# Kernel optimization log

Measured on AMD Instinct MI355X. Metric: run time of the kernel, lower is better.

## Reference

```python
import jax, jax.numpy as jnp
import numpy as np

N, E, D, H = 50000, 500000, 128, 8
DH = D // H  # per-head dim = int(out_dim // num_heads)
EPS_LN = 1e-5
EPS_BN = 1e-5


def _ln(x, g, b):
    m = x.mean(-1, keepdims=True)
    v = ((x - m) ** 2).mean(-1, keepdims=True)
    return (x - m) * jax.lax.rsqrt(v + EPS_LN) * g + b


def _bn(x, g, b):
    # BatchNorm1d, training-mode statistics (biased variance over the batch)
    m = x.mean(0)
    v = ((x - m) ** 2).mean(0)
    return (x - m) * jax.lax.rsqrt(v + EPS_BN) * g + b


def setup_inputs() -> dict:
    key = jax.random.key(0)
    ks = jax.random.split(key, 16)
    rn = lambda k, shape: (jax.random.normal(k, shape, jnp.float32) * 0.05)
    h = jax.random.normal(ks[0], (N, D), jnp.float32)
    src = jax.random.randint(ks[1], (E,), 0, N).astype(jnp.int32)
    # guarantee every node receives at least one message so z > 0 (no 0/0)
    dst = jnp.concatenate([jnp.arange(N, dtype=jnp.int32),
                           jax.random.randint(ks[2], (E - N,), 0, N).astype(jnp.int32)])
    return {
        "h": h, "src": src, "dst": dst,
        # per-node TransformerEncoder (seq_len == 1 subgraphs)
        "Win": rn(ks[3], (3 * D, D)), "bin": jnp.zeros((3 * D,), jnp.float32),
        "Wout": rn(ks[4], (D, D)), "bout": jnp.zeros((D,), jnp.float32),
        "Wte1": rn(ks[5], (4 * D, D)), "bte1": jnp.zeros((4 * D,), jnp.float32),
        "Wte2": rn(ks[6], (D, 4 * D)), "bte2": jnp.zeros((D,), jnp.float32),
        "ln1g": jnp.ones((D,), jnp.float32), "ln1b": jnp.zeros((D,), jnp.float32),
        "ln2g": jnp.ones((D,), jnp.float32), "ln2b": jnp.zeros((D,), jnp.float32),
        # graph multi-head attention projections (use_bias=False)
        "WQ": rn(ks[7], (D, D)), "WK": rn(ks[8], (D, D)), "WV": rn(ks[9], (D, D)),
        # node-wise FFN + batch norms
        "W1": rn(ks[10], (2 * D, D)), "b1": jnp.zeros((2 * D,), jnp.float32),
        "W2": rn(ks[11], (D, 2 * D)), "b2": jnp.zeros((D,), jnp.float32),
        "bn1g": jnp.ones((D,), jnp.float32), "bn1b": jnp.zeros((D,), jnp.float32),
        "bn2g": jnp.ones((D,), jnp.float32), "bn2b": jnp.zeros((D,), jnp.float32),
    }


def _forward(h, src, dst, Win, bin_, Wout, bout, Wte1, bte1, Wte2, bte2,
             ln1g, ln1b, ln2g, ln2b, WQ, WK, WV,
             W1, b1, W2, b2, bn1g, bn1b, bn2g, bn2b):
    # --- per-node TransformerEncoder. Each dgl.node_subgraph(g, [i]) contains
    # only the center node, so self-attention runs over a length-1 sequence:
    # softmax of a single score is 1, hence attn_out = out_proj(v).
    v = h @ Win[2 * D:].T + bin_[2 * D:]            # V slice of in_proj
    x = _ln(h + (v @ Wout.T + bout), ln1g, ln1b)
    ff = jax.nn.relu(x @ Wte1.T + bte1) @ Wte2.T + bte2
    hsub = _ln(x + ff, ln2g, ln2b)                  # [N, D]

    # --- graph multi-head attention (DGL apply_edges / send_and_recv)
    Qh = (hsub @ WQ.T).reshape(N, H, DH)
    Kh = (hsub @ WK.T).reshape(N, H, DH)
    Vh = (hsub @ WV.T).reshape(N, H, DH)
    score = (Kh[src] * Qh[dst]).sum(-1)             # [E, H]  K_src . Q_dst
    score = jnp.exp(jnp.clip(score / np.sqrt(DH), -5.0, 5.0))
    wV = jax.ops.segment_sum(Vh[src] * score[:, :, None], dst, num_segments=N)
    z = jax.ops.segment_sum(score, dst, num_segments=N)
    attn = (wV / z[:, :, None]).reshape(N, D)

    # --- residual + BN + FFN + residual + BN (dropout p=0 / eval mode)
    hh = _bn(hsub + attn, bn1g, bn1b)
    h_in2 = hh
    hh = jax.nn.relu(hh @ W1.T + b1) @ W2.T + b2
    return _bn(h_in2 + hh, bn2g, bn2b)


def reference(h, src, dst, Win, bin, Wout, bout, Wte1, bte1, Wte2, bte2,
              ln1g, ln1b, ln2g, ln2b, WQ, WK, WV,
              W1, b1, W2, b2, bn1g, bn1b, bn2g, bn2b):
    return _forward(h, src, dst, Win, bin, Wout, bout, Wte1, bte1, Wte2, bte2,
                    ln1g, ln1b, ln2g, ln2b, WQ, WK, WV,
                    W1, b1, W2, b2, bn1g, bn1b, bn2g, bn2b)
```

## Files before the change

kernel.cpp:

```cpp
#include <hip/hip_runtime.h>
#include <hip/hip_bf16.h>


#define D_ 128

typedef __attribute__((ext_vector_type(8))) short short8;
typedef __attribute__((ext_vector_type(4))) short short4v;
typedef __attribute__((ext_vector_type(4))) float f32x4;

__device__ __forceinline__ float b2f(ushort u) {
    union { uint u32; float f; } x; x.u32 = ((uint)u) << 16; return x.f;
}
__device__ __forceinline__ ushort f2b(float f) {
    union { __hip_bfloat16 h; ushort u; } v; v.h = __float2bfloat16(f); return v.u;
}

template<int AMODE, int EPI, bool RELU, bool RESF32>
__global__ __launch_bounds__(512) void gemm_bf16(
    const void* __restrict__ Aptr, const ushort* __restrict__ W,
    const float* __restrict__ bias, void* __restrict__ C,
    const float* __restrict__ bn_in, float* __restrict__ bn_out,
    const float* __restrict__ bng, const float* __restrict__ bnb,
    const void* __restrict__ resid, const ushort* __restrict__ y1res,
    const float* __restrict__ lng, const float* __restrict__ lnb,
    float invn, int n, int K, int M)
{
    __shared__ ushort Abuf[2][128 * 32];
    __shared__ ushort Bbuf[2][128 * 32];
    __shared__ float s_sh[128], t_sh[128];

    const int t    = threadIdx.x;
    const int lane = t & 63;
    const int w    = t >> 6;
    const int r0   = blockIdx.x * 128;
    const int c0   = blockIdx.y * 128;
    const int wr   = (w >> 1) * 32;
    const int wc   = (w & 1) * 64;
    const int rl   = lane & 15;
    const int kh   = lane >> 4;

    if (AMODE == 2 || EPI == 2) {
        if (t < 128) {
            float m   = bn_in[t] * invn;
            float var = bn_in[128 + t] * invn - m * m;
            float rs  = rsqrtf(var + 1e-5f);
            float s   = rs * bng[t];
            s_sh[t] = s;
            t_sh[t] = bnb[t] - m * s;
        }
        __syncthreads();
    }

    f32x4 acc[2][4] = {};
    const int nc = K >> 5;
    const int row = t >> 2, pos = t & 3;

    if (AMODE == 1) {
        for (int c = 0; c < nc; ++c) {
            int kc = c * 32;
            const int ch = pos;
            int gr = r0 + row;
            short8 aval = {};
            if (gr < n) {
                const float* Af = (const float*)Aptr;
                float4 f0 = *reinterpret_cast<const float4*>(Af + (size_t)gr * K + kc + ch * 8);
                float4 f1 = *reinterpret_cast<const float4*>(Af + (size_t)gr * K + kc + ch * 8 + 4);
                aval[0] = (short)f2b(f0.x); aval[1] = (short)f2b(f0.y);
                aval[2] = (short)f2b(f0.z); aval[3] = (short)f2b(f0.w);
                aval[4] = (short)f2b(f1.x); aval[5] = (short)f2b(f1.y);
                aval[6] = (short)f2b(f1.z); aval[7] = (short)f2b(f1.w);
            }
            short8 bval = *reinterpret_cast<const short8*>(W + (size_t)(c0 + row) * K + kc + ch * 8);
            __syncthreads();
            int sw = ch ^ ((row >> 1) & 3);
            *reinterpret_cast<short8*>(&Abuf[0][row * 32 + sw * 8]) = aval;
            *reinterpret_cast<short8*>(&Bbuf[0][row * 32 + sw * 8]) = bval;
            __syncthreads();
            short8 af[2], bfr[4];
            #pragma unroll
            for (int m = 0; m < 2; ++m) {
                int rr = wr + m * 16 + rl;
                af[m] = *reinterpret_cast<const short8*>(&Abuf[0][rr * 32 + (kh ^ ((rr >> 1) & 3)) * 8]);
            }
            #pragma unroll
            for (int nn = 0; nn < 4; ++nn) {
                int col = wc + nn * 16 + rl;
                bfr[nn] = *reinterpret_cast<const short8*>(&Bbuf[0][col * 32 + (kh ^ ((col >> 1) & 3)) * 8]);
            }
            #pragma unroll
            for (int m = 0; m < 2; ++m)
                #pragma unroll
                for (int nn = 0; nn < 4; ++nn)
                    acc[m][nn] = __builtin_amdgcn_mfma_f32_16x16x32_bf16(
                        bfr[nn], af[m], acc[m][nn], 0, 0, 0);
        }
    } else {
        const int ch = pos ^ ((row >> 1) & 3);
        const ushort* Abase = (const ushort*)Aptr + (size_t)(r0 + row) * K + ch * 8;
        const ushort* Bbase = W + (size_t)(c0 + row) * K + ch * 8;
        __builtin_amdgcn_global_load_lds(
            (const __attribute__((address_space(1))) void*)Abase,
            (__attribute__((address_space(3))) void*)&Abuf[0][t * 8], 16, 0, 0);
        __builtin_amdgcn_global_load_lds(
            (const __attribute__((address_space(1))) void*)Bbase,
            (__attribute__((address_space(3))) void*)&Bbuf[0][t * 8], 16, 0, 0);
        __syncthreads();
        for (int c = 0; c < nc; ++c) {
            if (c + 1 < nc) {
                int half = (c + 1) & 1;
                __builtin_amdgcn_global_load_lds(
                    (const __attribute__((address_space(1))) void*)(Abase + (c + 1) * 32),
                    (__attribute__((address_space(3))) void*)&Abuf[half][t * 8], 16, 0, 0);
                __builtin_amdgcn_global_load_lds(
                    (const __attribute__((address_space(1))) void*)(Bbase + (c + 1) * 32),
                    (__attribute__((address_space(3))) void*)&Bbuf[half][t * 8], 16, 0, 0);
            }
            const int cur = c & 1;
            const int kc  = c * 32;
            short8 af[2], bfr[4];
            #pragma unroll
            for (int m = 0; m < 2; ++m) {
                int rr = wr + m * 16 + rl;
                af[m] = *reinterpret_cast<const short8*>(&Abuf[cur][rr * 32 + (kh ^ ((rr >> 1) & 3)) * 8]);
            }
            if (AMODE == 2) {
                #pragma unroll
                for (int m = 0; m < 2; ++m) {
                    short8 v = af[m];
                    #pragma unroll
                    for (int q = 0; q < 8; ++q) {
                        int cch = kc + kh * 8 + q;
                        v[q] = (short)f2b(fmaf(b2f((ushort)v[q]), s_sh[cch], t_sh[cch]));
                    }
                    af[m] = v;
                }
            }
            #pragma unroll
            for (int nn = 0; nn < 4; ++nn) {
                int col = wc + nn * 16 + rl;
                bfr[nn] = *reinterpret_cast<const short8*>(&Bbuf[cur][col * 32 + (kh ^ ((col >> 1) & 3)) * 8]);
            }
            #pragma unroll
            for (int m = 0; m < 2; ++m)
                #pragma unroll
                for (int nn = 0; nn < 4; ++nn)
                    acc[m][nn] = __builtin_amdgcn_mfma_f32_16x16x32_bf16(
                        bfr[nn], af[m], acc[m][nn], 0, 0, 0);
            __syncthreads();
        }
    }

    const int ch4 = kh * 4;

    if (EPI == 1) {
        __shared__ float lnS[128][2], lnS2[128][2];
        float4 bb[4];
        #pragma unroll
        for (int nn = 0; nn < 4; ++nn)
            bb[nn] = *reinterpret_cast<const float4*>(bias + wc + nn * 16 + ch4);
        #pragma unroll
        for (int m = 0; m < 2; ++m) {
            int r = r0 + wr + m * 16 + rl;
            float s = 0.f, s2 = 0.f;
            #pragma unroll
            for (int nn = 0; nn < 4; ++nn) {
                int c = wc + nn * 16 + ch4;
                float rv[4] = {0.f, 0.f, 0.f, 0.f};
                if (r < n) {
                    if (RESF32) {
                        float4 f = *reinterpret_cast<const float4*>((const float*)resid + (size_t)r * 128 + c);
                        rv[0] = f.x; rv[1] = f.y; rv[2] = f.z; rv[3] = f.w;
                    } else {
                        short4v f = *reinterpret_cast<const short4v*>((const ushort*)resid + (size_t)r * 128 + c);
                        rv[0] = b2f((ushort)f[0]); rv[1] = b2f((ushort)f[1]);
                        rv[2] = b2f((ushort)f[2]); rv[3] = b2f((ushort)f[3]);
                    }
                }
                float bj[4] = {bb[nn].x, bb[nn].y, bb[nn].z, bb[nn].w};
                #pragma unroll
                for (int j = 0; j < 4; ++j) {
                    float o = acc[m][nn][j] + bj[j] + rv[j];
                    acc[m][nn][j] = o;
                    s += o; s2 += o * o;
                }
            }
            s  += __shfl_xor(s, 16);  s  += __shfl_xor(s, 32);
            s2 += __shfl_xor(s2, 16); s2 += __shfl_xor(s2, 32);
            if (kh == 0) {
                lnS[wr + m * 16 + rl][w & 1]  = s;
                lnS2[wr + m * 16 + rl][w & 1] = s2;
            }
        }
        __syncthreads();
        #pragma unroll
        for (int m = 0; m < 2; ++m) {
            int rloc = wr + m * 16 + rl;
            int r = r0 + rloc;
            float S  = lnS[rloc][0] + lnS[rloc][1];
            float S2 = lnS2[rloc][0] + lnS2[rloc][1];
            float mean = S * (1.f / 128.f);
            float var  = S2 * (1.f / 128.f) - mean * mean;
            float rs   = rsqrtf(var + 1e-5f);
            if (r >= n) continue;
            #pragma unroll
            for (int nn = 0; nn < 4; ++nn) {
                int c = wc + nn * 16 + ch4;
                float4 gv = *reinterpret_cast<const float4*>(lng + c);
                float4 bv = *reinterpret_cast<const float4*>(lnb + c);
                float gj[4] = {gv.x, gv.y, gv.z, gv.w};
                float bj[4] = {bv.x, bv.y, bv.z, bv.w};
                short4v p;
                #pragma unroll
                for (int j = 0; j < 4; ++j)
                    p[j] = (short)f2b((acc[m][nn][j] - mean) * rs * gj[j] + bj[j]);
                *reinterpret_cast<short4v*>((ushort*)C + (size_t)r * 128 + c) = p;
            }
        }
        return;
    }

    if (EPI == 2) {
        __shared__ float csum[128], csum2[128];
        if (t < 128) { csum[t] = 0.f; csum2[t] = 0.f; }
        __syncthreads();
        float ps[4][4] = {};
        float ps2[4][4] = {};
        #pragma unroll
        for (int m = 0; m < 2; ++m) {
            int r = r0 + wr + m * 16 + rl;
            bool ok = r < n;
            #pragma unroll
            for (int nn = 0; nn < 4; ++nn) {
                int c = wc + nn * 16 + ch4;
                float4 bb = *reinterpret_cast<const float4*>(bias + c);
                float bj[4] = {bb.x, bb.y, bb.z, bb.w};
                short4v yv = {};
                if (ok) yv = *reinterpret_cast<const short4v*>(y1res + (size_t)r * 128 + c);
                short4v p;
                #pragma unroll
                for (int j = 0; j < 4; ++j) {
                    float o = 0.f;
                    if (ok) {
                        o = acc[m][nn][j] + bj[j]
                          + fmaf(b2f((ushort)yv[j]), s_sh[c + j], t_sh[c + j]);
                    }
                    ps[nn][j] += o; ps2[nn][j] += o * o;
                    p[j] = (short)f2b(o);
                }
                if (ok)
                    *reinterpret_cast<short4v*>((ushort*)C + (size_t)r * 128 + c) = p;
            }
        }
        #pragma unroll
        for (int nn = 0; nn < 4; ++nn)
            #pragma unroll
            for (int j = 0; j < 4; ++j) {
                float a = ps[nn][j], b = ps2[nn][j];
                #pragma unroll
                for (int o2 = 1; o2 < 16; o2 <<= 1) {
                    a += __shfl_xor(a, o2);
                    b += __shfl_xor(b, o2);
                }
                if (rl == 0) {
                    int c = wc + nn * 16 + ch4 + j;
                    atomicAdd(&csum[c], a);
                    atomicAdd(&csum2[c], b);
                }
            }
        __syncthreads();
        if (t < 128) {
            atomicAdd(bn_out + t, csum[t]);
            atomicAdd(bn_out + 128 + t, csum2[t]);
        }
        return;
    }

    #pragma unroll
    for (int m = 0; m < 2; ++m) {
        int r = r0 + wr + m * 16 + rl;
        if (r >= n) continue;
        #pragma unroll
        for (int nn = 0; nn < 4; ++nn) {
            int c = c0 + wc + nn * 16 + ch4;
            f32x4 vacc = acc[m][nn];
            float4 bb = make_float4(0.f, 0.f, 0.f, 0.f);
            if (bias) bb = *reinterpret_cast<const float4*>(bias + c);
            float o0 = vacc[0] + bb.x, o1 = vacc[1] + bb.y;
            float o2 = vacc[2] + bb.z, o3 = vacc[3] + bb.w;
            if (RELU) {
                o0 = fmaxf(o0, 0.f); o1 = fmaxf(o1, 0.f);
                o2 = fmaxf(o2, 0.f); o3 = fmaxf(o3, 0.f);
            }
            short4v p;
            p[0] = (short)f2b(o0); p[1] = (short)f2b(o1);
            p[2] = (short)f2b(o2); p[3] = (short)f2b(o3);
            *reinterpret_cast<short4v*>((ushort*)C + (size_t)r * M + c) = p;
        }
    }
}

__global__ __launch_bounds__(256) void zero_kernel(int4* __restrict__ p, int n4)
{
    int i = blockIdx.x * blockDim.x + threadIdx.x;
    int stride = gridDim.x * blockDim.x;
    int4 z = make_int4(0, 0, 0, 0);
    for (; i < n4; i += stride) p[i] = z;
}

__global__ void hist_kernel(const int* __restrict__ dst, int* __restrict__ cnt, int E_)
{
    int e = blockIdx.x * blockDim.x + threadIdx.x;
    if (e < E_) atomicAdd(cnt + dst[e], 1);
}

__global__ __launch_bounds__(256) void scan_block_kernel(
    int* __restrict__ data, int* __restrict__ bsum, int n)
{
    __shared__ int tmp[256];
    int i = blockIdx.x * 256 + threadIdx.x;
    int v = (i < n) ? data[i] : 0;
    tmp[threadIdx.x] = v;
    __syncthreads();
    #pragma unroll
    for (int o = 1; o < 256; o <<= 1) {
        int y = (threadIdx.x >= o) ? tmp[threadIdx.x - o] : 0;
        __syncthreads();
        tmp[threadIdx.x] += y;
        __syncthreads();
    }
    if (i < n) data[i] = tmp[threadIdx.x] - v;
    if (threadIdx.x == 255) bsum[blockIdx.x] = tmp[255];
}

__global__ __launch_bounds__(256) void add_off_kernel(
    int* __restrict__ data, const int* __restrict__ bsum, int n, int nb)
{
    __shared__ int red[4];
    int b = blockIdx.x;
    int v = (threadIdx.x < b && threadIdx.x < nb) ? bsum[threadIdx.x] : 0;
    #pragma unroll
    for (int o = 1; o < 64; o <<= 1) v += __shfl_xor(v, o);
    if ((threadIdx.x & 63) == 0) red[threadIdx.x >> 6] = v;
    __syncthreads();
    int off = red[0] + red[1] + red[2] + red[3];
    int i = b * 256 + threadIdx.x;
    if (i < n) data[i] += off;
}

__global__ void scatter_kernel(const int* __restrict__ src, const int* __restrict__ dst,
                               int* __restrict__ rowptr, int* __restrict__ csr_src, int E_)
{
    int e = blockIdx.x * blockDim.x + threadIdx.x;
    if (e >= E_) return;
    int pos = atomicAdd(rowptr + dst[e], 1);
    csr_src[pos] = src[e];
}

__global__ __launch_bounds__(256) void attn_agg_kernel(
    const int* __restrict__ rowptr, const int* __restrict__ csr_src,
    const ushort* __restrict__ QKV, const ushort* __restrict__ hsub,
    ushort* __restrict__ out, int n)
{
    int node  = (blockIdx.x * blockDim.x + threadIdx.x) >> 5;
    int lane5 = threadIdx.x & 31;
    int slot  = lane5 >> 3;
    int hd    = lane5 & 7;
    bool valid = node < n;
    int nd = valid ? node : 0;
    int start = (valid && nd) ? rowptr[nd - 1] : 0;
    int end   = valid ? rowptr[nd] : 0;

    const ushort* qp = QKV + (size_t)nd * 384 + hd * 16;
    short8 q0 = *reinterpret_cast<const short8*>(qp);
    short8 q1 = *reinterpret_cast<const short8*>(qp + 8);
    float q[16];
    #pragma unroll
    for (int i = 0; i < 8; ++i) { q[i] = b2f((ushort)q0[i]); q[8 + i] = b2f((ushort)q1[i]); }

    float acc[16] = {};
    float zh = 0.f;
    for (int j = start; j < end; j += 4) {
        int idx = j + slot;
        if (idx < end) {
            int s = csr_src[idx];
            const ushort* kp = QKV + (size_t)s * 384 + 128 + hd * 16;
            short8 k0 = *reinterpret_cast<const short8*>(kp);
            short8 k1 = *reinterpret_cast<const short8*>(kp + 8);
            float p = 0.f;
            #pragma unroll
            for (int i = 0; i < 8; ++i) {
                p = fmaf(b2f((ushort)k0[i]), q[i], p);
                p = fmaf(b2f((ushort)k1[i]), q[8 + i], p);
            }
            float sc = __expf(fminf(fmaxf(p * 0.25f, -5.f), 5.f));
            short8 v0 = *reinterpret_cast<const short8*>(kp + 128);
            short8 v1 = *reinterpret_cast<const short8*>(kp + 136);
            #pragma unroll
            for (int i = 0; i < 8; ++i) {
                acc[i]     = fmaf(sc, b2f((ushort)v0[i]), acc[i]);
                acc[8 + i] = fmaf(sc, b2f((ushort)v1[i]), acc[8 + i]);
            }
            zh += sc;
        }
    }
    #pragma unroll
    for (int i = 0; i < 16; ++i) {
        acc[i] += __shfl_xor(acc[i], 8);
        acc[i] += __shfl_xor(acc[i], 16);
    }
    zh += __shfl_xor(zh, 8);
    zh += __shfl_xor(zh, 16);

    if (slot == 0 && valid) {
        const ushort* hp = hsub + (size_t)nd * D_ + hd * 16;
        short8 h0 = *reinterpret_cast<const short8*>(hp);
        short8 h1 = *reinterpret_cast<const short8*>(hp + 8);
        float inv = 1.f / zh;
        short8 o0, o1;
        #pragma unroll
        for (int i = 0; i < 8; ++i) {
            o0[i] = (short)f2b(b2f((ushort)h0[i]) + acc[i] * inv);
            o1[i] = (short)f2b(b2f((ushort)h1[i]) + acc[8 + i] * inv);
        }
        ushort* op = out + (size_t)nd * D_ + hd * 16;
        *reinterpret_cast<short8*>(op)     = o0;
        *reinterpret_cast<short8*>(op + 8) = o1;
    }
}

__global__ __launch_bounds__(256) void bn_stats_kernel(
    const ushort* __restrict__ x, float* __restrict__ sums, int n)
{
    int c    = threadIdx.x & 127;
    int half = threadIdx.x >> 7;
    float s = 0.f, s2 = 0.f;
    for (int r = blockIdx.x * 2 + half; r < n; r += gridDim.x * 2) {
        float v = b2f(x[(size_t)r * D_ + c]);
        s += v; s2 += v * v;
    }
    __shared__ float ls[256], ls2[256];
    ls[threadIdx.x] = s; ls2[threadIdx.x] = s2;
    __syncthreads();
    if (half == 0) {
        s  += ls[threadIdx.x + 128];
        s2 += ls2[threadIdx.x + 128];
        atomicAdd(sums + c, s);
        atomicAdd(sums + 128 + c, s2);
    }
}

__global__ void bn_norm_kernel(const ushort* __restrict__ x,
                               const float* __restrict__ stats,
                               const float* __restrict__ g, const float* __restrict__ b,
                               float* __restrict__ out, float invn, int total4)
{
    int i = blockIdx.x * blockDim.x + threadIdx.x;
    if (i >= total4) return;
    int cb = (i << 2) & 127;
    short4v v = reinterpret_cast<const short4v*>(x)[i];
    float4 o;
    float r[4];
    #pragma unroll
    for (int q = 0; q < 4; ++q) {
        int c = cb + q;
        float m   = stats[c] * invn;
        float var = stats[128 + c] * invn - m * m;
        float rs  = rsqrtf(var + 1e-5f);
        r[q] = (b2f((ushort)v[q]) - m) * rs * g[c] + b[c];
    }
    o.x = r[0]; o.y = r[1]; o.z = r[2]; o.w = r[3];
    reinterpret_cast<float4*>(out)[i] = o;
}

struct WPtrs { const float* p[7]; };

__global__ __launch_bounds__(256) void prep_w_kernel(
    const float* __restrict__ Win, const float* __restrict__ bin_,
    const float* __restrict__ Wout, const float* __restrict__ bout,
    WPtrs wp, ushort* __restrict__ wbf, float* __restrict__ bfused)
{
    int b = blockIdx.x;
    if (b < 64) {
        int idx = b * 256 + threadIdx.x;
        int i = idx >> 7, c = idx & 127;
        const float* WinV = Win + 256 * 128;
        float s = 0.f;
        for (int j = 0; j < 128; ++j)
            s = fmaf(Wout[i * 128 + j], WinV[j * 128 + c], s);
        wbf[245760 + idx] = f2b(s);
        if (c == 0) {
            float tb = bout[i];
            for (int j = 0; j < 128; ++j)
                tb = fmaf(Wout[i * 128 + j], bin_[256 + j], tb);
            bfused[i] = tb;
        }
    } else {
        const int off[8] = {0, 65536, 131072, 147456, 163840, 180224, 212992, 245760};
        int e0 = ((b - 64) * 256 + threadIdx.x) * 4;
        if (e0 >= 245760) return;
        int s = 0;
        #pragma unroll
        for (int j = 1; j < 7; ++j) if (e0 >= off[j]) s = j;
        float4 f = *reinterpret_cast<const float4*>(wp.p[s] + (e0 - off[s]));
        short4v o;
        o[0] = (short)f2b(f.x); o[1] = (short)f2b(f.y);
        o[2] = (short)f2b(f.z); o[3] = (short)f2b(f.w);
        *reinterpret_cast<short4v*>(wbf + e0) = o;
    }
}

extern "C" void kernel_launch(void* const* d_in, const int* in_sizes, int n_in,
                              void* d_out, int out_size, void* d_ws, size_t ws_size,
                              hipStream_t stream)
{
    const float* h    = (const float*)d_in[0];
    const int*   src  = (const int*)d_in[1];
    const int*   dst  = (const int*)d_in[2];
    const float* Win  = (const float*)d_in[3];
    const float* bin_ = (const float*)d_in[4];
    const float* Wout = (const float*)d_in[5];
    const float* bout = (const float*)d_in[6];
    const float* Wte1 = (const float*)d_in[7];
    const float* bte1 = (const float*)d_in[8];
    const float* Wte2 = (const float*)d_in[9];
    const float* bte2 = (const float*)d_in[10];
    const float* ln1g = (const float*)d_in[11];
    const float* ln1b = (const float*)d_in[12];
    const float* ln2g = (const float*)d_in[13];
    const float* ln2b = (const float*)d_in[14];
    const float* WQ   = (const float*)d_in[15];
    const float* WK   = (const float*)d_in[16];
    const float* WV   = (const float*)d_in[17];
    const float* W1   = (const float*)d_in[18];
    const float* b1   = (const float*)d_in[19];
    const float* W2   = (const float*)d_in[20];
    const float* b2   = (const float*)d_in[21];
    const float* bn1g = (const float*)d_in[22];
    const float* bn1b = (const float*)d_in[23];
    const float* bn2g = (const float*)d_in[24];
    const float* bn2b = (const float*)d_in[25];

    const int N_ = in_sizes[0] / D_;
    const int E_ = in_sizes[1];
    const size_t S2 = (size_t)N_ * D_ / 2;

    float* ws = (float*)d_ws;
    size_t off_tail = 7 * S2;
    size_t need = (off_tail + 131072 + 128 + 512) * sizeof(float)
                + (size_t)(N_ + E_ + 256) * sizeof(int) + 4096;
    if (ws_size < need) return;

    ushort* bufA   = (ushort*)ws;
    ushort* bufB   = (ushort*)(ws + S2);
    ushort* bufC   = (ushort*)(ws + 2 * S2);
    ushort* bufD   = (ushort*)(ws + 3 * S2);
    ushort* wbf    = (ushort*)(ws + off_tail);
    float*  bfused = ws + off_tail + 131072;
    float*  stats  = bfused + 128;
    int* rowptr  = (int*)(stats + 512);
    int* csr_src = rowptr + N_;
    int* bsum    = csr_src + E_;

    const ushort* Wte1_bf = wbf;
    const ushort* Wte2_bf = wbf + 65536;
    const ushort* WQKV_bf = wbf + 131072;
    const ushort* W1_bf   = wbf + 180224;
    const ushort* W2_bf   = wbf + 212992;
    ushort*       Wf_bf   = wbf + 245760;

    dim3 blk(256);
    dim3 blk512(512);
    const int rowBlocks = (N_ + 127) / 128;
    const int totElems  = N_ * D_;
    const dim3 gNode((N_ + 7) / 8);
    const int nb = (N_ + 255) / 256;
    const float invn = 1.f / (float)N_;

    {
        int n4 = (512 + N_) / 4;
        int zblocks = (n4 + 255) / 256;
        if (zblocks > 128) zblocks = 128;
        zero_kernel<<<dim3(zblocks), blk, 0, stream>>>((int4*)stats, n4);
    }

    hist_kernel<<<dim3((E_ + 255) / 256), blk, 0, stream>>>(dst, rowptr, E_);
    scan_block_kernel<<<dim3(nb), blk, 0, stream>>>(rowptr, bsum, N_);
    add_off_kernel<<<dim3(nb), blk, 0, stream>>>(rowptr, bsum, N_, nb);
    scatter_kernel<<<dim3((E_ + 255) / 256), blk, 0, stream>>>(src, dst, rowptr, csr_src, E_);

    WPtrs wp;
    wp.p[0] = Wte1; wp.p[1] = Wte2; wp.p[2] = WQ; wp.p[3] = WK; wp.p[4] = WV;
    wp.p[5] = W1;   wp.p[6] = W2;
    prep_w_kernel<<<dim3(304), blk, 0, stream>>>(Win, bin_, Wout, bout, wp, wbf, bfused);

    gemm_bf16<1, 1, false, true><<<dim3(rowBlocks, 1), blk512, 0, stream>>>(
        h, Wf_bf, bfused, bufA, nullptr, nullptr, nullptr, nullptr,
        h, nullptr, ln1g, ln1b, 0.f, N_, 128, 128);
    gemm_bf16<0, 0, true, false><<<dim3(rowBlocks, 4), blk512, 0, stream>>>(
        bufA, Wte1_bf, bte1, bufD, nullptr, nullptr, nullptr, nullptr,
        nullptr, nullptr, nullptr, nullptr, 0.f, N_, 128, 512);
    gemm_bf16<0, 1, false, false><<<dim3(rowBlocks, 1), blk512, 0, stream>>>(
        bufD, Wte2_bf, bte2, bufC, nullptr, nullptr, nullptr, nullptr,
        bufA, nullptr, ln2g, ln2b, 0.f, N_, 512, 128);

    gemm_bf16<0, 0, false, false><<<dim3(rowBlocks, 3), blk512, 0, stream>>>(
        bufC, WQKV_bf, nullptr, bufD, nullptr, nullptr, nullptr, nullptr,
        nullptr, nullptr, nullptr, nullptr, 0.f, N_, 128, 384);
    attn_agg_kernel<<<gNode, blk, 0, stream>>>(
        rowptr, csr_src, bufD, bufC, bufA, N_);

    bn_stats_kernel<<<dim3(512), blk, 0, stream>>>(bufA, stats, N_);

    gemm_bf16<2, 0, true, false><<<dim3(rowBlocks, 2), blk512, 0, stream>>>(
        bufA, W1_bf, b1, bufD, stats, nullptr, bn1g, bn1b,
        nullptr, nullptr, nullptr, nullptr, invn, N_, 128, 256);
    gemm_bf16<0, 2, false, false><<<dim3(rowBlocks, 1), blk512, 0, stream>>>(
        bufD, W2_bf, b2, bufB, stats, stats + 256, bn1g, bn1b,
        nullptr, bufA, nullptr, nullptr, invn, N_, 256, 128);
    bn_norm_kernel<<<dim3((totElems / 4 + 255) / 256), blk, 0, stream>>>(
        bufB, stats + 256, bn2g, bn2b, (float*)d_out, invn, totElems / 4);
}
```

Measured before the change: 276.1 us.

## Fuse transformer FFN up/down GEMMs with residual LayerNorm in one kernel

Replaces the two-GEMM transformer feed-forward (128->512 with ReLU, then 512->128 with residual + LayerNorm) with one kernel. Each 128-row block keeps its input tile in LDS and computes the hidden layer in 64-column chunks, feeding each chunk straight into the second GEMM accumulator. Weight chunks are double-buffered through async global-to-LDS loads. This removes the write and re-read of the 50000x512 bf16 intermediate and one launch. In exchange it needs large LDS per block, lowering occupancy, and adds two barriers per chunk.

```diff
diff --git a/kernel.cpp b/kernel.cpp
--- a/kernel.cpp
+++ b/kernel.cpp
@@ -295,6 +295,204 @@
             p[0] = (short)f2b(o0); p[1] = (short)f2b(o1);
             p[2] = (short)f2b(o2); p[3] = (short)f2b(o3);
             *reinterpret_cast<short4v*>((ushort*)C + (size_t)r * M + c) = p;
+        }
+    }
+}
+
+__global__ __launch_bounds__(512) void ffn_ln_kernel(
+    const ushort* __restrict__ X,   const ushort* __restrict__ W1g,
+    const ushort* __restrict__ W2g,
+    const float* __restrict__ b1v,  const float* __restrict__ b2v,
+    const float* __restrict__ lng,  const float* __restrict__ lnb,
+    ushort* __restrict__ out, int n)
+{
+    __shared__ ushort Xs[128 * 128];
+    __shared__ ushort FF1[128 * 64];
+    __shared__ ushort W1s[2][64 * 128];
+    __shared__ ushort W2s[2][128 * 64];
+    __shared__ float lnS[128][2], lnS2[128][2];
+
+    const int t    = threadIdx.x;
+    const int lane = t & 63;
+    const int w    = t >> 6;
+    const int r0   = blockIdx.x * 128;
+    const int rl   = lane & 15;
+    const int kh   = lane >> 4;
+    const int wr   = (w >> 1) * 32;
+    const int wc1  = (w & 1) * 32;
+    const int wc2  = (w & 1) * 64;
+
+    #pragma unroll
+    for (int i = 0; i < 4; ++i) {
+        int s = t + i * 512;
+        int row = s >> 4, pos = s & 15;
+        int srcch = pos ^ ((row >> 1) & 7);
+        if (r0 + row < n)
+            __builtin_amdgcn_global_load_lds(
+                (const __attribute__((address_space(1))) void*)(X + (size_t)(r0 + row) * 128 + srcch * 8),
+                (__attribute__((address_space(3))) void*)&Xs[s * 8], 16, 0, 0);
+    }
+    #pragma unroll
+    for (int i = 0; i < 2; ++i) {
+        int s = t + i * 512;
+        int row = s >> 4, pos = s & 15;
+        int srcch = pos ^ ((row >> 1) & 7);
+        __builtin_amdgcn_global_load_lds(
+            (const __attribute__((address_space(1))) void*)(W1g + (size_t)row * 128 + srcch * 8),
+            (__attribute__((address_space(3))) void*)&W1s[0][s * 8], 16, 0, 0);
+    }
+    #pragma unroll
+    for (int i = 0; i < 2; ++i) {
+        int s = t + i * 512;
+        int row = s >> 3, pos = s & 7;
+        int srcch = pos ^ ((row >> 1) & 7);
+        __builtin_amdgcn_global_load_lds(
+            (const __attribute__((address_space(1))) void*)(W2g + (size_t)row * 512 + srcch * 8),
+            (__attribute__((address_space(3))) void*)&W2s[0][s * 8], 16, 0, 0);
+    }
+    __syncthreads();
+
+    f32x4 acc2[2][4] = {};
+
+    for (int c = 0; c < 8; ++c) {
+        const int cur = c & 1, nxt = cur ^ 1;
+        if (c < 7) {
+            #pragma unroll
+            for (int i = 0; i < 2; ++i) {
+                int s = t + i * 512;
+                int row = s >> 4, pos = s & 15;
+                int srcch = pos ^ ((row >> 1) & 7);
+                __builtin_amdgcn_global_load_lds(
+                    (const __attribute__((address_space(1))) void*)(W1g + (size_t)((c + 1) * 64 + row) * 128 + srcch * 8),
+                    (__attribute__((address_space(3))) void*)&W1s[nxt][s * 8], 16, 0, 0);
+            }
+            #pragma unroll
+            for (int i = 0; i < 2; ++i) {
+                int s = t + i * 512;
+                int row = s >> 3, pos = s & 7;
+                int srcch = pos ^ ((row >> 1) & 7);
+                __builtin_amdgcn_global_load_lds(
+                    (const __attribute__((address_space(1))) void*)(W2g + (size_t)row * 512 + (c + 1) * 64 + srcch * 8),
+                    (__attribute__((address_space(3))) void*)&W2s[nxt][s * 8], 16, 0, 0);
+            }
+        }
+        f32x4 acc1[2][2] = {};
+        #pragma unroll
+        for (int ks = 0; ks < 4; ++ks) {
+            short8 af[2], bf[2];
+            #pragma unroll
+            for (int m = 0; m < 2; ++m) {
+                int row = wr + m * 16 + rl;
+                int chn = ks * 4 + kh;
+                af[m] = *reinterpret_cast<const short8*>(&Xs[row * 128 + (chn ^ ((row >> 1) & 7)) * 8]);
+            }
+            #pragma unroll
+            for (int nn = 0; nn < 2; ++nn) {
+                int colL = wc1 + nn * 16 + rl;
+                int chn = ks * 4 + kh;
+                bf[nn] = *reinterpret_cast<const short8*>(&W1s[cur][colL * 128 + (chn ^ ((colL >> 1) & 7)) * 8]);
+            }
+            #pragma unroll
+            for (int m = 0; m < 2; ++m)
+                #pragma unroll
+                for (int nn = 0; nn < 2; ++nn)
+                    acc1[m][nn] = __builtin_amdgcn_mfma_f32_16x16x32_bf16(
+                        bf[nn], af[m], acc1[m][nn], 0, 0, 0);
+        }
+        #pragma unroll
+        for (int m = 0; m < 2; ++m) {
+            int row = wr + m * 16 + rl;
+            #pragma unroll
+            for (int nn = 0; nn < 2; ++nn) {
+                int colL = wc1 + nn * 16 + kh * 4;
+                float4 bb = *reinterpret_cast<const float4*>(b1v + c * 64 + colL);
+                short4v p;
+                p[0] = (short)f2b(fmaxf(acc1[m][nn][0] + bb.x, 0.f));
+                p[1] = (short)f2b(fmaxf(acc1[m][nn][1] + bb.y, 0.f));
+                p[2] = (short)f2b(fmaxf(acc1[m][nn][2] + bb.z, 0.f));
+                p[3] = (short)f2b(fmaxf(acc1[m][nn][3] + bb.w, 0.f));
+                int chn = colL >> 3;
+                *reinterpret_cast<short4v*>(
+                    &FF1[row * 64 + (chn ^ ((row >> 1) & 7)) * 8 + (kh & 1) * 4]) = p;
+            }
+        }
+        __syncthreads();
+
+        #pragma unroll
+        for (int ks = 0; ks < 2; ++ks) {
+            short8 af[2], bf[4];
+            #pragma unroll
+            for (int m = 0; m < 2; ++m) {
+                int row = wr + m * 16 + rl;
+                int chn = ks * 4 + kh;
+                af[m] = *reinterpret_cast<const short8*>(&FF1[row * 64 + (chn ^ ((row >> 1) & 7)) * 8]);
+            }
+            #pragma unroll
+            for (int nn = 0; nn < 4; ++nn) {
+                int col = wc2 + nn * 16 + rl;
+                int chn = ks * 4 + kh;
+                bf[nn] = *reinterpret_cast<const short8*>(&W2s[cur][col * 64 + (chn ^ ((col >> 1) & 7)) * 8]);
+            }
+            #pragma unroll
+            for (int m = 0; m < 2; ++m)
+                #pragma unroll
+                for (int nn = 0; nn < 4; ++nn)
+                    acc2[m][nn] = __builtin_amdgcn_mfma_f32_16x16x32_bf16(
+                        bf[nn], af[m], acc2[m][nn], 0, 0, 0);
+        }
+        __syncthreads();
+    }
+
+    const int ch4 = kh * 4;
+    #pragma unroll
+    for (int m = 0; m < 2; ++m) {
+        int rloc = wr + m * 16 + rl;
+        float s = 0.f, s2 = 0.f;
+        #pragma unroll
+        for (int nn = 0; nn < 4; ++nn) {
+            int col = wc2 + nn * 16 + ch4;
+            int chn = col >> 3;
+            short4v xv = *reinterpret_cast<const short4v*>(
+                &Xs[rloc * 128 + (chn ^ ((rloc >> 1) & 7)) * 8 + (kh & 1) * 4]);
+            float4 bb = *reinterpret_cast<const float4*>(b2v + col);
+            float bj[4] = {bb.x, bb.y, bb.z, bb.w};
+            #pragma unroll
+            for (int j = 0; j < 4; ++j) {
+                float o = acc2[m][nn][j] + bj[j] + b2f((ushort)xv[j]);
+                acc2[m][nn][j] = o;
+                s += o; s2 += o * o;
+            }
+        }
+        s  += __shfl_xor(s, 16);  s  += __shfl_xor(s, 32);
+        s2 += __shfl_xor(s2, 16); s2 += __shfl_xor(s2, 32);
+        if (kh == 0) {
+            lnS[rloc][w & 1]  = s;
+            lnS2[rloc][w & 1] = s2;
+        }
+    }
+    __syncthreads();
+    #pragma unroll
+    for (int m = 0; m < 2; ++m) {
+        int rloc = wr + m * 16 + rl;
+        int r = r0 + rloc;
+        float S  = lnS[rloc][0] + lnS[rloc][1];
+        float S2 = lnS2[rloc][0] + lnS2[rloc][1];
+        float mean = S * (1.f / 128.f);
+        float var  = S2 * (1.f / 128.f) - mean * mean;
+        float rs   = rsqrtf(var + 1e-5f);
+        if (r >= n) continue;
+        #pragma unroll
+        for (int nn = 0; nn < 4; ++nn) {
+            int col = wc2 + nn * 16 + ch4;
+            float4 gv = *reinterpret_cast<const float4*>(lng + col);
+            float4 bv = *reinterpret_cast<const float4*>(lnb + col);
+            float gj[4] = {gv.x, gv.y, gv.z, gv.w};
+            float bj[4] = {bv.x, bv.y, bv.z, bv.w};
+            short4v p;
+            #pragma unroll
+            for (int j = 0; j < 4; ++j)
+                p[j] = (short)f2b((acc2[m][nn][j] - mean) * rs * gj[j] + bj[j]);
+            *reinterpret_cast<short4v*>(out + (size_t)r * 128 + col) = p;
         }
     }
 }
@@ -596,12 +794,8 @@
     gemm_bf16<1, 1, false, true><<<dim3(rowBlocks, 1), blk512, 0, stream>>>(
         h, Wf_bf, bfused, bufA, nullptr, nullptr, nullptr, nullptr,
         h, nullptr, ln1g, ln1b, 0.f, N_, 128, 128);
-    gemm_bf16<0, 0, true, false><<<dim3(rowBlocks, 4), blk512, 0, stream>>>(
-        bufA, Wte1_bf, bte1, bufD, nullptr, nullptr, nullptr, nullptr,
-        nullptr, nullptr, nullptr, nullptr, 0.f, N_, 128, 512);
-    gemm_bf16<0, 1, false, false><<<dim3(rowBlocks, 1), blk512, 0, stream>>>(
-        bufD, Wte2_bf, bte2, bufC, nullptr, nullptr, nullptr, nullptr,
-        bufA, nullptr, ln2g, ln2b, 0.f, N_, 512, 128);
+    ffn_ln_kernel<<<dim3(rowBlocks), blk512, 0, stream>>>(
+        bufA, Wte1_bf, Wte2_bf, bte1, bte2, ln2g, ln2b, bufC, N_);
 
     gemm_bf16<0, 0, false, false><<<dim3(rowBlocks, 3), blk512, 0, stream>>>(
         bufC, WQKV_bf, nullptr, bufD, nullptr, nullptr, nullptr, nullptr,
```

Result: faster. 257.9 us (-6.6%).
